# Performance work log

Measured on AMD Instinct MI355X. Metric: run time of the kernel, lower is better.

Reference implementation:

```python
import jax, jax.numpy as jnp
import numpy as np

EMBED_TIME = 128
NUM_HEADS = 4
INPUT_DIM = 64
NHIDDEN = 256
B, LQ, LK = 4, 256, 512


def setup_inputs() -> dict:
    key = jax.random.key(0)
    ks = jax.random.split(key, 8)
    scale = np.float32(0.05)
    return {
        "query": jax.random.normal(ks[0], (B, LQ, EMBED_TIME), jnp.float32),
        "key_ts": jax.random.normal(ks[1], (B, LK, EMBED_TIME), jnp.float32),
        "value": jax.random.normal(ks[2], (B, LK, INPUT_DIM), jnp.float32),
        "mask": jax.random.randint(ks[3], (B, LK, INPUT_DIM), 0, 2, jnp.int32),
        # params stored [in, out] (transpose of torch nn.Linear convention)
        "Wq": jax.random.normal(ks[4], (EMBED_TIME, EMBED_TIME), jnp.float32) * scale,
        "bq": jnp.zeros((EMBED_TIME,), jnp.float32),
        "Wk": jax.random.normal(ks[5], (EMBED_TIME, EMBED_TIME), jnp.float32) * scale,
        "bk": jnp.zeros((EMBED_TIME,), jnp.float32),
        "W3": jax.random.normal(ks[6], (INPUT_DIM * NUM_HEADS, NHIDDEN), jnp.float32) * scale,
        "b3": jnp.zeros((NHIDDEN,), jnp.float32),
    }


def reference(query, key_ts, value, mask, Wq, bq, Wk, bk, W3, b3):
    b, lk, d = value.shape  # B, Lk, input_dim
    h = NUM_HEADS
    dk = EMBED_TIME // h
    # project & split heads: [B, L, E] -> [B, h, L, dk]
    q = (query @ Wq + bq).reshape(b, -1, h, dk).transpose(0, 2, 1, 3)
    k = (key_ts @ Wk + bk).reshape(b, -1, h, dk).transpose(0, 2, 1, 3)
    # scaled dot-product time scores: [B, h, Lq, Lk]
    scores = jnp.einsum('bhqe,bhke->bhqk', q, k) / np.float32(np.sqrt(dk))
    # broadcast scores over value feature dim, mask per feature: [B, h, Lq, Lk, D]
    scores = jnp.where(mask[:, None, None, :, :] == 0, jnp.float32(-1e9), scores[..., None])
    # softmax over key (time) axis, per feature
    p_attn = jax.nn.softmax(scores, axis=-2)
    # elementwise weighted reduce over Lk: [B, h, Lq, D]
    x = jnp.einsum('bhqkd,bkd->bhqd', p_attn, value)
    x = x.transpose(0, 2, 1, 3).reshape(b, -1, h * d)  # [B, Lq, h*D]
    # replicate reinitialize_dim: permute input columns of last layer by descending L1 norm
    perm = jnp.argsort(-jnp.sum(jnp.abs(W3), axis=1))
    return x @ W3[perm] + b3
```

## Files before the change

kernel.cpp:

```cpp
#include <hip/hip_runtime.h>
#include <math.h>

#define ETIME 128
#define NHEADS 4
#define DK 32
#define DIN 64
#define NHID 256
#define BB 4
#define LQg 256
#define LKg 512
#define KC 128
#define KCN 4
#define QT 16

__global__ __launch_bounds__(256) void prep_all(
    const float* __restrict__ query, const float* __restrict__ key_ts,
    const float* __restrict__ Wq, const float* __restrict__ bq,
    const float* __restrict__ Wk, const float* __restrict__ bk,
    const float* __restrict__ value, const int* __restrict__ mask,
    const float* __restrict__ W3,
    float* __restrict__ qbuf, float* __restrict__ kbuf,
    float2* __restrict__ vmbuf, float* __restrict__ sbuf)
{
    __shared__ float in_lds[8][ETIME];
    __shared__ float red[4];
    const int t = threadIdx.x;
    const int blk = blockIdx.x;

    if (blk < 384) {
        const int r0 = blk * 8;
        const bool is_q = (r0 < BB * LQg);
        const float* in   = is_q ? (query + (size_t)r0 * ETIME)
                                 : (key_ts + (size_t)(r0 - BB * LQg) * ETIME);
        const float* W    = is_q ? Wq : Wk;
        const float* bias = is_q ? bq : bk;
        float* outp       = is_q ? (qbuf + (size_t)r0 * ETIME)
                                 : (kbuf + (size_t)(r0 - BB * LQg) * ETIME);

        reinterpret_cast<float4*>(&in_lds[0][0])[t] =
            reinterpret_cast<const float4*>(in)[t];
        __syncthreads();

        const int j4 = t & 31;
        const int row = t >> 5;
        const float4* W4 = reinterpret_cast<const float4*>(W);
        float4 acc = make_float4(0.f, 0.f, 0.f, 0.f);
#pragma unroll 8
        for (int i = 0; i < ETIME; ++i) {
            const float4 w = W4[i * 32 + j4];
            const float xv = in_lds[row][i];
            acc.x = fmaf(xv, w.x, acc.x);
            acc.y = fmaf(xv, w.y, acc.y);
            acc.z = fmaf(xv, w.z, acc.z);
            acc.w = fmaf(xv, w.w, acc.w);
        }
        const float4 bb = reinterpret_cast<const float4*>(bias)[j4];
        acc.x += bb.x; acc.y += bb.y; acc.z += bb.z; acc.w += bb.w;
        reinterpret_cast<float4*>(outp + row * ETIME)[j4] = acc;
    } else if (blk < 640) {
        const int i = (blk - 384) * 256 + t;
        for (int idx = i; idx < BB * LKg * DIN; idx += 256 * 256) {
            const float mf = (float)mask[idx];
            vmbuf[idx] = make_float2(mf, value[idx] * mf);
        }
    } else {
        const int row = blk - 640;
        float a = fabsf(W3[(size_t)row * NHID + t]);
#pragma unroll
        for (int off = 32; off; off >>= 1) a += __shfl_xor(a, off, 64);
        if ((t & 63) == 0) red[t >> 6] = a;
        __syncthreads();
        if (t == 0) sbuf[row] = red[0] + red[1] + red[2] + red[3];
    }
}

__global__ __launch_bounds__(256, 4) void attn_chunk(
    const float* __restrict__ qbuf, const float* __restrict__ kbuf,
    const float2* __restrict__ vmbuf, float2* __restrict__ pbuf)
{
    __shared__ float qlds[QT][DK];
    __shared__ float S[QT][KC];

    const int t = threadIdx.x;
    int bid = blockIdx.x;
    bid = (bid & 7) * 128 + (bid >> 3);
    const int kc = bid & 3;
    const int qt = (bid >> 2) & 15;
    const int h  = (bid >> 6) & 3;
    const int b  = bid >> 8;
    const int qbase = qt * QT;
    const int kbase = kc * KC;

    if (t < 128) {
        const int q = t >> 3, j = t & 7;
        float4 v = reinterpret_cast<const float4*>(
            qbuf + (size_t)(b * LQg + qbase + q) * ETIME + h * DK)[j];
        const float rsq = 0.17677669529663687f;
        v.x *= rsq; v.y *= rsq; v.z *= rsq; v.w *= rsq;
        reinterpret_cast<float4*>(&qlds[q][0])[j] = v;
    }
    __syncthreads();

    {
        const int k = t & 127;
        const int qg = t >> 7;
        const float* krow = kbuf + (size_t)(b * LKg + kbase + k) * ETIME + h * DK;
        float4 kr[8];
#pragma unroll
        for (int i = 0; i < 8; ++i)
            kr[i] = reinterpret_cast<const float4*>(krow)[i];
        float acc[8] = {0, 0, 0, 0, 0, 0, 0, 0};
#pragma unroll
        for (int i4 = 0; i4 < 8; ++i4) {
            const float4 kv = kr[i4];
#pragma unroll
            for (int jj = 0; jj < 8; ++jj) {
                const float4 qv =
                    reinterpret_cast<const float4*>(&qlds[qg * 8 + jj][0])[i4];
                acc[jj] = fmaf(qv.x, kv.x, acc[jj]);
                acc[jj] = fmaf(qv.y, kv.y, acc[jj]);
                acc[jj] = fmaf(qv.z, kv.z, acc[jj]);
                acc[jj] = fmaf(qv.w, kv.w, acc[jj]);
            }
        }
#pragma unroll
        for (int jj = 0; jj < 8; ++jj)
            S[qg * 8 + jj][k] = __expf(acc[jj]);
    }
    __syncthreads();

    {
        const int d = t & 63;
        const int w = t >> 6;
        float num[4] = {0, 0, 0, 0}, den[4] = {0, 0, 0, 0};
        const float2* vp = vmbuf + (size_t)(b * LKg + kbase) * DIN + d;
#pragma unroll 4
        for (int k4 = 0; k4 < KC / 4; ++k4) {
            float2 vm[4];
#pragma unroll
            for (int u = 0; u < 4; ++u) vm[u] = vp[(size_t)(k4 * 4 + u) * DIN];
#pragma unroll
            for (int jj = 0; jj < 4; ++jj) {
                const float4 e4 =
                    reinterpret_cast<const float4*>(&S[w * 4 + jj][0])[k4];
                num[jj] = fmaf(e4.x, vm[0].y, num[jj]); den[jj] = fmaf(e4.x, vm[0].x, den[jj]);
                num[jj] = fmaf(e4.y, vm[1].y, num[jj]); den[jj] = fmaf(e4.y, vm[1].x, den[jj]);
                num[jj] = fmaf(e4.z, vm[2].y, num[jj]); den[jj] = fmaf(e4.z, vm[2].x, den[jj]);
                num[jj] = fmaf(e4.w, vm[3].y, num[jj]); den[jj] = fmaf(e4.w, vm[3].x, den[jj]);
            }
        }
#pragma unroll
        for (int jj = 0; jj < 4; ++jj) {
            const int q = qbase + w * 4 + jj;
            pbuf[((size_t)((b * NHEADS + h) * LQg + q) * KCN + kc) * DIN + d] =
                make_float2(den[jj], num[jj]);
        }
    }
}

__global__ __launch_bounds__(256) void out_fused(
    const float2* __restrict__ pbuf, const float* __restrict__ W3,
    const float* __restrict__ b3, const float* __restrict__ sbuf,
    float* __restrict__ out)
{
    __shared__ float s_lds[NHID];
    __shared__ float xraw[4][NHID];
    __shared__ float x2[4][NHID];
    const int t = threadIdx.x;
    const int r0 = blockIdx.x * 4;
    const int b = r0 >> 8;
    const int q0 = r0 & 255;
    const int h = t >> 6, d = t & 63;

    s_lds[t] = sbuf[t];
#pragma unroll
    for (int r = 0; r < 4; ++r) {
        const float2* pp =
            pbuf + ((size_t)((b * NHEADS + h) * LQg + q0 + r) * KCN) * DIN + d;
        float num = 0.f, den = 0.f;
#pragma unroll
        for (int kc = 0; kc < KCN; ++kc) {
            const float2 v = pp[kc * DIN];
            den += v.x; num += v.y;
        }
        xraw[r][t] = num / den;
    }
    __syncthreads();

    const float si = s_lds[t];
    int rank = 0;
#pragma unroll 8
    for (int j = 0; j < NHID; ++j) {
        const float sj = s_lds[j];
        rank += (sj > si) || (sj == si && j < t);
    }
#pragma unroll
    for (int r = 0; r < 4; ++r) x2[r][t] = xraw[r][rank];
    __syncthreads();

    float acc[4] = {0, 0, 0, 0};
#pragma unroll 4
    for (int c4 = 0; c4 < NHID / 4; ++c4) {
        const float w0 = W3[(size_t)(c4 * 4 + 0) * NHID + t];
        const float w1 = W3[(size_t)(c4 * 4 + 1) * NHID + t];
        const float w2 = W3[(size_t)(c4 * 4 + 2) * NHID + t];
        const float w3 = W3[(size_t)(c4 * 4 + 3) * NHID + t];
#pragma unroll
        for (int r = 0; r < 4; ++r) {
            const float4 xv = reinterpret_cast<const float4*>(&x2[r][0])[c4];
            acc[r] = fmaf(xv.x, w0, acc[r]);
            acc[r] = fmaf(xv.y, w1, acc[r]);
            acc[r] = fmaf(xv.z, w2, acc[r]);
            acc[r] = fmaf(xv.w, w3, acc[r]);
        }
    }
    const float bn = b3[t];
#pragma unroll
    for (int r = 0; r < 4; ++r) out[(size_t)(r0 + r) * NHID + t] = acc[r] + bn;
}

extern "C" void kernel_launch(void* const* d_in, const int* in_sizes, int n_in,
                              void* d_out, int out_size, void* d_ws, size_t ws_size,
                              hipStream_t stream) {
    const float* query  = (const float*)d_in[0];
    const float* key_ts = (const float*)d_in[1];
    const float* value  = (const float*)d_in[2];
    const int*   mask   = (const int*)d_in[3];
    const float* Wq     = (const float*)d_in[4];
    const float* bq     = (const float*)d_in[5];
    const float* Wk     = (const float*)d_in[6];
    const float* bk     = (const float*)d_in[7];
    const float* W3     = (const float*)d_in[8];
    const float* b3     = (const float*)d_in[9];
    float* out = (float*)d_out;

    char* ws = (char*)d_ws;
    float*  qbuf  = (float*) (ws);
    float*  kbuf  = (float*) (ws + (512u  << 10));
    float2* vmbuf = (float2*)(ws + (1536u << 10));
    float2* pbuf  = (float2*)(ws + (2560u << 10));
    float*  sbuf  = (float*) (ws + (10752u << 10));

    prep_all<<<896, 256, 0, stream>>>(query, key_ts, Wq, bq, Wk, bk,
                                      value, mask, W3, qbuf, kbuf, vmbuf, sbuf);
    attn_chunk<<<BB * NHEADS * QT * KCN, 256, 0, stream>>>(qbuf, kbuf, vmbuf, pbuf);
    out_fused<<<BB * LQg / 4, 256, 0, stream>>>(pbuf, W3, b3, sbuf, out);
}
```

Baseline: 51.43 us.

## Head-major q/k layout, LDS-staged keys, split-K value reduce, tiled output GEMM

The prep kernel now writes q and k projections in a head-major [B,H,L,DK] layout, so attention blocks read contiguous tiles. Those blocks stage keys through padded LDS. The value reduction is reorganised so each wave owns 32 keys across all 16 queries, and the partial sums are combined in shared memory before one store. The output kernel moves to 512 threads, stages W3 through LDS in 32-row tiles with register prefetch, and computes two rows per thread. Costs are higher register pressure in attn_chunk (occupancy hint drops to 3) and more LDS use.

```diff
diff --git a/kernel.cpp b/kernel.cpp
--- a/kernel.cpp
+++ b/kernel.cpp
@@ -34,8 +34,6 @@
                                  : (key_ts + (size_t)(r0 - BB * LQg) * ETIME);
         const float* W    = is_q ? Wq : Wk;
         const float* bias = is_q ? bq : bk;
-        float* outp       = is_q ? (qbuf + (size_t)r0 * ETIME)
-                                 : (kbuf + (size_t)(r0 - BB * LQg) * ETIME);
 
         reinterpret_cast<float4*>(&in_lds[0][0])[t] =
             reinterpret_cast<const float4*>(in)[t];
@@ -56,7 +54,17 @@
         }
         const float4 bb = reinterpret_cast<const float4*>(bias)[j4];
         acc.x += bb.x; acc.y += bb.y; acc.z += bb.z; acc.w += bb.w;
-        reinterpret_cast<float4*>(outp + row * ETIME)[j4] = acc;
+
+        const int h = j4 >> 3, dd = (j4 & 7) * 4;
+        float* dst;
+        if (is_q) {
+            const int gr = r0 + row, b = gr >> 8, q = gr & 255;
+            dst = qbuf + ((size_t)((b * NHEADS + h) * LQg + q)) * DK + dd;
+        } else {
+            const int gr = r0 - BB * LQg + row, b = gr >> 9, k = gr & 511;
+            dst = kbuf + ((size_t)((b * NHEADS + h) * LKg + k)) * DK + dd;
+        }
+        *reinterpret_cast<float4*>(dst) = acc;
     } else if (blk < 640) {
         const int i = (blk - 384) * 256 + t;
         for (int idx = i; idx < BB * LKg * DIN; idx += 256 * 256) {
@@ -74,12 +82,15 @@
     }
 }
 
-__global__ __launch_bounds__(256, 4) void attn_chunk(
+__global__ __launch_bounds__(256, 3) void attn_chunk(
     const float* __restrict__ qbuf, const float* __restrict__ kbuf,
     const float2* __restrict__ vmbuf, float2* __restrict__ pbuf)
 {
+    __shared__ float smem[4 * QT * DIN * 2];
+    __shared__ float S[QT][KC];
     __shared__ float qlds[QT][DK];
-    __shared__ float S[QT][KC];
+    float (*klds)[33] = reinterpret_cast<float(*)[33]>(smem);
+    float2 (*xpart)[QT][DIN] = reinterpret_cast<float2(*)[QT][DIN]>(smem);
 
     const int t = threadIdx.x;
     int bid = blockIdx.x;
@@ -92,35 +103,43 @@
     const int kbase = kc * KC;
 
     if (t < 128) {
-        const int q = t >> 3, j = t & 7;
         float4 v = reinterpret_cast<const float4*>(
-            qbuf + (size_t)(b * LQg + qbase + q) * ETIME + h * DK)[j];
+            qbuf + ((size_t)((b * NHEADS + h) * LQg + qbase)) * DK)[t];
         const float rsq = 0.17677669529663687f;
         v.x *= rsq; v.y *= rsq; v.z *= rsq; v.w *= rsq;
-        reinterpret_cast<float4*>(&qlds[q][0])[j] = v;
+        reinterpret_cast<float4*>(&qlds[t >> 3][0])[t & 7] = v;
+    }
+    {
+        const float4* ksrc = reinterpret_cast<const float4*>(
+            kbuf + ((size_t)((b * NHEADS + h) * LKg + kbase)) * DK);
+#pragma unroll
+        for (int u = 0; u < 4; ++u) {
+            const int idx4 = t + u * 256;
+            const float4 v = ksrc[idx4];
+            const int k = idx4 >> 3, c = (idx4 & 7) * 4;
+            klds[k][c + 0] = v.x; klds[k][c + 1] = v.y;
+            klds[k][c + 2] = v.z; klds[k][c + 3] = v.w;
+        }
     }
     __syncthreads();
 
     {
         const int k = t & 127;
         const int qg = t >> 7;
-        const float* krow = kbuf + (size_t)(b * LKg + kbase + k) * ETIME + h * DK;
-        float4 kr[8];
-#pragma unroll
-        for (int i = 0; i < 8; ++i)
-            kr[i] = reinterpret_cast<const float4*>(krow)[i];
+        float kr[DK];
+#pragma unroll
+        for (int i = 0; i < DK; ++i) kr[i] = klds[k][i];
         float acc[8] = {0, 0, 0, 0, 0, 0, 0, 0};
 #pragma unroll
         for (int i4 = 0; i4 < 8; ++i4) {
-            const float4 kv = kr[i4];
 #pragma unroll
             for (int jj = 0; jj < 8; ++jj) {
                 const float4 qv =
                     reinterpret_cast<const float4*>(&qlds[qg * 8 + jj][0])[i4];
-                acc[jj] = fmaf(qv.x, kv.x, acc[jj]);
-                acc[jj] = fmaf(qv.y, kv.y, acc[jj]);
-                acc[jj] = fmaf(qv.z, kv.z, acc[jj]);
-                acc[jj] = fmaf(qv.w, kv.w, acc[jj]);
+                acc[jj] = fmaf(qv.x, kr[i4 * 4 + 0], acc[jj]);
+                acc[jj] = fmaf(qv.y, kr[i4 * 4 + 1], acc[jj]);
+                acc[jj] = fmaf(qv.z, kr[i4 * 4 + 2], acc[jj]);
+                acc[jj] = fmaf(qv.w, kr[i4 * 4 + 3], acc[jj]);
             }
         }
 #pragma unroll
@@ -132,33 +151,37 @@
     {
         const int d = t & 63;
         const int w = t >> 6;
-        float num[4] = {0, 0, 0, 0}, den[4] = {0, 0, 0, 0};
-        const float2* vp = vmbuf + (size_t)(b * LKg + kbase) * DIN + d;
-#pragma unroll 4
-        for (int k4 = 0; k4 < KC / 4; ++k4) {
-            float2 vm[4];
-#pragma unroll
-            for (int u = 0; u < 4; ++u) vm[u] = vp[(size_t)(k4 * 4 + u) * DIN];
-#pragma unroll
-            for (int jj = 0; jj < 4; ++jj) {
-                const float4 e4 =
-                    reinterpret_cast<const float4*>(&S[w * 4 + jj][0])[k4];
-                num[jj] = fmaf(e4.x, vm[0].y, num[jj]); den[jj] = fmaf(e4.x, vm[0].x, den[jj]);
-                num[jj] = fmaf(e4.y, vm[1].y, num[jj]); den[jj] = fmaf(e4.y, vm[1].x, den[jj]);
-                num[jj] = fmaf(e4.z, vm[2].y, num[jj]); den[jj] = fmaf(e4.z, vm[2].x, den[jj]);
-                num[jj] = fmaf(e4.w, vm[3].y, num[jj]); den[jj] = fmaf(e4.w, vm[3].x, den[jj]);
+        const float2* vp = vmbuf + ((size_t)(b * LKg + kbase + w * 32)) * DIN + d;
+        float2 vm[32];
+#pragma unroll
+        for (int u = 0; u < 32; ++u) vm[u] = vp[(size_t)u * DIN];
+#pragma unroll 2
+        for (int q = 0; q < QT; ++q) {
+            const float4* Sq = reinterpret_cast<const float4*>(&S[q][w * 32]);
+            float num = 0.f, den = 0.f;
+#pragma unroll
+            for (int k4 = 0; k4 < 8; ++k4) {
+                const float4 e = Sq[k4];
+                num = fmaf(e.x, vm[k4 * 4 + 0].y, num); den = fmaf(e.x, vm[k4 * 4 + 0].x, den);
+                num = fmaf(e.y, vm[k4 * 4 + 1].y, num); den = fmaf(e.y, vm[k4 * 4 + 1].x, den);
+                num = fmaf(e.z, vm[k4 * 4 + 2].y, num); den = fmaf(e.z, vm[k4 * 4 + 2].x, den);
+                num = fmaf(e.w, vm[k4 * 4 + 3].y, num); den = fmaf(e.w, vm[k4 * 4 + 3].x, den);
             }
-        }
-#pragma unroll
-        for (int jj = 0; jj < 4; ++jj) {
-            const int q = qbase + w * 4 + jj;
-            pbuf[((size_t)((b * NHEADS + h) * LQg + q) * KCN + kc) * DIN + d] =
-                make_float2(den[jj], num[jj]);
-        }
-    }
-}
-
-__global__ __launch_bounds__(256) void out_fused(
+            xpart[w][q][d] = make_float2(den, num);
+        }
+    }
+    __syncthreads();
+
+    for (int e = t; e < QT * DIN; e += 256) {
+        const int q = e >> 6, d = e & 63;
+        const float2 p0 = xpart[0][q][d], p1 = xpart[1][q][d];
+        const float2 p2 = xpart[2][q][d], p3 = xpart[3][q][d];
+        pbuf[((size_t)((b * NHEADS + h) * LQg + qbase + q) * KCN + kc) * DIN + d] =
+            make_float2(p0.x + p1.x + p2.x + p3.x, p0.y + p1.y + p2.y + p3.y);
+    }
+}
+
+__global__ __launch_bounds__(512) void out_fused(
     const float2* __restrict__ pbuf, const float* __restrict__ W3,
     const float* __restrict__ b3, const float* __restrict__ sbuf,
     float* __restrict__ out)
@@ -166,15 +189,18 @@
     __shared__ float s_lds[NHID];
     __shared__ float xraw[4][NHID];
     __shared__ float x2[4][NHID];
+    __shared__ float W3l[32][NHID];
     const int t = threadIdx.x;
     const int r0 = blockIdx.x * 4;
     const int b = r0 >> 8;
     const int q0 = r0 & 255;
-    const int h = t >> 6, d = t & 63;
-
-    s_lds[t] = sbuf[t];
-#pragma unroll
-    for (int r = 0; r < 4; ++r) {
+
+    if (t < NHID) s_lds[t] = sbuf[t];
+#pragma unroll
+    for (int u = 0; u < 2; ++u) {
+        const int e = t + u * 512;
+        const int r = e >> 8, c = e & 255;
+        const int h = c >> 6, d = c & 63;
         const float2* pp =
             pbuf + ((size_t)((b * NHEADS + h) * LQg + q0 + r) * KCN) * DIN + d;
         float num = 0.f, den = 0.f;
@@ -183,40 +209,57 @@
             const float2 v = pp[kc * DIN];
             den += v.x; num += v.y;
         }
-        xraw[r][t] = num / den;
-    }
-    __syncthreads();
-
-    const float si = s_lds[t];
-    int rank = 0;
+        xraw[r][c] = num / den;
+    }
+    __syncthreads();
+
+    if (t < NHID) {
+        const float si = s_lds[t];
+        int rank = 0;
 #pragma unroll 8
-    for (int j = 0; j < NHID; ++j) {
-        const float sj = s_lds[j];
-        rank += (sj > si) || (sj == si && j < t);
-    }
-#pragma unroll
-    for (int r = 0; r < 4; ++r) x2[r][t] = xraw[r][rank];
-    __syncthreads();
-
-    float acc[4] = {0, 0, 0, 0};
-#pragma unroll 4
-    for (int c4 = 0; c4 < NHID / 4; ++c4) {
-        const float w0 = W3[(size_t)(c4 * 4 + 0) * NHID + t];
-        const float w1 = W3[(size_t)(c4 * 4 + 1) * NHID + t];
-        const float w2 = W3[(size_t)(c4 * 4 + 2) * NHID + t];
-        const float w3 = W3[(size_t)(c4 * 4 + 3) * NHID + t];
-#pragma unroll
-        for (int r = 0; r < 4; ++r) {
-            const float4 xv = reinterpret_cast<const float4*>(&x2[r][0])[c4];
-            acc[r] = fmaf(xv.x, w0, acc[r]);
-            acc[r] = fmaf(xv.y, w1, acc[r]);
-            acc[r] = fmaf(xv.z, w2, acc[r]);
-            acc[r] = fmaf(xv.w, w3, acc[r]);
-        }
-    }
-    const float bn = b3[t];
-#pragma unroll
-    for (int r = 0; r < 4; ++r) out[(size_t)(r0 + r) * NHID + t] = acc[r] + bn;
+        for (int j = 0; j < NHID; ++j) {
+            const float sj = s_lds[j];
+            rank += (sj > si) || (sj == si && j < t);
+        }
+#pragma unroll
+        for (int r = 0; r < 4; ++r) x2[r][t] = xraw[r][rank];
+    }
+
+    const int n = t & 255, rh = t >> 8;
+    const float4* W3g4 = reinterpret_cast<const float4*>(W3);
+    float4 pf[4];
+#pragma unroll
+    for (int u = 0; u < 4; ++u) pf[u] = W3g4[t + u * 512];
+    float acc0 = 0.f, acc1 = 0.f;
+
+    for (int kt = 0; kt < 8; ++kt) {
+        __syncthreads();
+#pragma unroll
+        for (int u = 0; u < 4; ++u)
+            reinterpret_cast<float4*>(&W3l[0][0])[t + u * 512] = pf[u];
+        if (kt < 7) {
+#pragma unroll
+            for (int u = 0; u < 4; ++u)
+                pf[u] = W3g4[(kt + 1) * 2048 + t + u * 512];
+        }
+        __syncthreads();
+#pragma unroll
+        for (int c4 = 0; c4 < 8; ++c4) {
+            const float4 xa = *reinterpret_cast<const float4*>(&x2[2 * rh][kt * 32 + c4 * 4]);
+            const float4 xb = *reinterpret_cast<const float4*>(&x2[2 * rh + 1][kt * 32 + c4 * 4]);
+            const float w0 = W3l[c4 * 4 + 0][n];
+            const float w1 = W3l[c4 * 4 + 1][n];
+            const float w2 = W3l[c4 * 4 + 2][n];
+            const float w3 = W3l[c4 * 4 + 3][n];
+            acc0 = fmaf(xa.x, w0, acc0); acc1 = fmaf(xb.x, w0, acc1);
+            acc0 = fmaf(xa.y, w1, acc0); acc1 = fmaf(xb.y, w1, acc1);
+            acc0 = fmaf(xa.z, w2, acc0); acc1 = fmaf(xb.z, w2, acc1);
+            acc0 = fmaf(xa.w, w3, acc0); acc1 = fmaf(xb.w, w3, acc1);
+        }
+    }
+    const float bn = b3[n];
+    out[(size_t)(r0 + 2 * rh + 0) * NHID + n] = acc0 + bn;
+    out[(size_t)(r0 + 2 * rh + 1) * NHID + n] = acc1 + bn;
 }
 
 extern "C" void kernel_launch(void* const* d_in, const int* in_sizes, int n_in,
@@ -244,5 +287,5 @@
     prep_all<<<896, 256, 0, stream>>>(query, key_ts, Wq, bq, Wk, bk,
                                       value, mask, W3, qbuf, kbuf, vmbuf, sbuf);
     attn_chunk<<<BB * NHEADS * QT * KCN, 256, 0, stream>>>(qbuf, kbuf, vmbuf, pbuf);
-    out_fused<<<BB * LQg / 4, 256, 0, stream>>>(pbuf, W3, b3, sbuf, out);
-}
+    out_fused<<<BB * LQg / 4, 512, 0, stream>>>(pbuf, W3, b3, sbuf, out);
+}
```

Measured after the change: 62.16 us. +20.9%, slower.

## Bit-pack mask, halve key chunk, stage K in LDS, split output GEMV

Applied to the files above, without the earlier changes.

The mask is packed into 64-bit ballot words and value is pre-masked, which replaces the float2 value/mask buffer and cuts the bytes read in the attention reduce. The key chunk shrinks from 128 to 64, doubling the attention grid to 2048 blocks, and K rows are staged in padded LDS. The value loads are software-prefetched one step ahead. The output kernel moves to 512 threads that split the hidden reduction in half and combine the halves through LDS, at the cost of a larger partial buffer and more partial sums to reduce.

```diff
diff --git a/kernel.cpp b/kernel.cpp
--- a/kernel.cpp
+++ b/kernel.cpp
@@ -9,9 +9,11 @@
 #define BB 4
 #define LQg 256
 #define LKg 512
-#define KC 128
-#define KCN 4
+#define KC 64
+#define KCN 8
 #define QT 16
+
+typedef unsigned long long ull;
 
 __global__ __launch_bounds__(256) void prep_all(
     const float* __restrict__ query, const float* __restrict__ key_ts,
@@ -20,7 +22,7 @@
     const float* __restrict__ value, const int* __restrict__ mask,
     const float* __restrict__ W3,
     float* __restrict__ qbuf, float* __restrict__ kbuf,
-    float2* __restrict__ vmbuf, float* __restrict__ sbuf)
+    float* __restrict__ valm, ull* __restrict__ mbits, float* __restrict__ sbuf)
 {
     __shared__ float in_lds[8][ETIME];
     __shared__ float red[4];
@@ -58,10 +60,16 @@
         acc.x += bb.x; acc.y += bb.y; acc.z += bb.z; acc.w += bb.w;
         reinterpret_cast<float4*>(outp + row * ETIME)[j4] = acc;
     } else if (blk < 640) {
-        const int i = (blk - 384) * 256 + t;
-        for (int idx = i; idx < BB * LKg * DIN; idx += 256 * 256) {
-            const float mf = (float)mask[idx];
-            vmbuf[idx] = make_float2(mf, value[idx] * mf);
+        const int lane = t & 63;
+        const int wgid = (blk - 384) * 4 + (t >> 6);
+#pragma unroll
+        for (int u = 0; u < 2; ++u) {
+            const int p = wgid * 2 + u;
+            const int idx = p * 64 + lane;
+            const int m = mask[idx];
+            valm[idx] = m ? value[idx] : 0.f;
+            const ull bits = __ballot(m != 0);
+            if (lane == 0) mbits[p] = bits;
         }
     } else {
         const int row = blk - 640;
@@ -76,18 +84,20 @@
 
 __global__ __launch_bounds__(256, 4) void attn_chunk(
     const float* __restrict__ qbuf, const float* __restrict__ kbuf,
-    const float2* __restrict__ vmbuf, float2* __restrict__ pbuf)
+    const float* __restrict__ valm, const ull* __restrict__ mbits,
+    float2* __restrict__ pbuf)
 {
     __shared__ float qlds[QT][DK];
+    __shared__ float klds[KC][DK + 1];
     __shared__ float S[QT][KC];
 
     const int t = threadIdx.x;
     int bid = blockIdx.x;
-    bid = (bid & 7) * 128 + (bid >> 3);
-    const int kc = bid & 3;
-    const int qt = (bid >> 2) & 15;
-    const int h  = (bid >> 6) & 3;
-    const int b  = bid >> 8;
+    bid = (bid & 7) * 256 + (bid >> 3);
+    const int kc = bid & 7;
+    const int qt = (bid >> 3) & 15;
+    const int h  = (bid >> 7) & 3;
+    const int b  = bid >> 9;
     const int qbase = qt * QT;
     const int kbase = kc * KC;
 
@@ -99,33 +109,42 @@
         v.x *= rsq; v.y *= rsq; v.z *= rsq; v.w *= rsq;
         reinterpret_cast<float4*>(&qlds[q][0])[j] = v;
     }
-    __syncthreads();
-
     {
-        const int k = t & 127;
-        const int qg = t >> 7;
-        const float* krow = kbuf + (size_t)(b * LKg + kbase + k) * ETIME + h * DK;
-        float4 kr[8];
-#pragma unroll
-        for (int i = 0; i < 8; ++i)
-            kr[i] = reinterpret_cast<const float4*>(krow)[i];
-        float acc[8] = {0, 0, 0, 0, 0, 0, 0, 0};
+#pragma unroll
+        for (int u = 0; u < 2; ++u) {
+            const int idx4 = t + u * 256;
+            const int k = idx4 >> 3, c = idx4 & 7;
+            const float4 v = reinterpret_cast<const float4*>(
+                kbuf + (size_t)(b * LKg + kbase + k) * ETIME + h * DK)[c];
+            klds[k][c * 4 + 0] = v.x; klds[k][c * 4 + 1] = v.y;
+            klds[k][c * 4 + 2] = v.z; klds[k][c * 4 + 3] = v.w;
+        }
+    }
+    __syncthreads();
+
+    {
+        const int k = t & 63;
+        const int qg = t >> 6;
+        float acc[4] = {0, 0, 0, 0};
 #pragma unroll
         for (int i4 = 0; i4 < 8; ++i4) {
-            const float4 kv = kr[i4];
-#pragma unroll
-            for (int jj = 0; jj < 8; ++jj) {
+            float kr0 = klds[k][i4 * 4 + 0];
+            float kr1 = klds[k][i4 * 4 + 1];
+            float kr2 = klds[k][i4 * 4 + 2];
+            float kr3 = klds[k][i4 * 4 + 3];
+#pragma unroll
+            for (int jj = 0; jj < 4; ++jj) {
                 const float4 qv =
-                    reinterpret_cast<const float4*>(&qlds[qg * 8 + jj][0])[i4];
-                acc[jj] = fmaf(qv.x, kv.x, acc[jj]);
-                acc[jj] = fmaf(qv.y, kv.y, acc[jj]);
-                acc[jj] = fmaf(qv.z, kv.z, acc[jj]);
-                acc[jj] = fmaf(qv.w, kv.w, acc[jj]);
+                    reinterpret_cast<const float4*>(&qlds[qg * 4 + jj][0])[i4];
+                acc[jj] = fmaf(qv.x, kr0, acc[jj]);
+                acc[jj] = fmaf(qv.y, kr1, acc[jj]);
+                acc[jj] = fmaf(qv.z, kr2, acc[jj]);
+                acc[jj] = fmaf(qv.w, kr3, acc[jj]);
             }
         }
 #pragma unroll
-        for (int jj = 0; jj < 8; ++jj)
-            S[qg * 8 + jj][k] = __expf(acc[jj]);
+        for (int jj = 0; jj < 4; ++jj)
+            S[qg * 4 + jj][k] = __expf(acc[jj]);
     }
     __syncthreads();
 
@@ -133,21 +152,34 @@
         const int d = t & 63;
         const int w = t >> 6;
         float num[4] = {0, 0, 0, 0}, den[4] = {0, 0, 0, 0};
-        const float2* vp = vmbuf + (size_t)(b * LKg + kbase) * DIN + d;
-#pragma unroll 4
+        const float* vp = valm + (size_t)(b * LKg + kbase) * DIN + d;
+        const ull*   mp = mbits + b * LKg + kbase;
+        float vcur[4], vnxt[4];
+#pragma unroll
+        for (int u = 0; u < 4; ++u) vcur[u] = vp[(size_t)u * DIN];
         for (int k4 = 0; k4 < KC / 4; ++k4) {
-            float2 vm[4];
-#pragma unroll
-            for (int u = 0; u < 4; ++u) vm[u] = vp[(size_t)(k4 * 4 + u) * DIN];
+            if (k4 < KC / 4 - 1) {
+#pragma unroll
+                for (int u = 0; u < 4; ++u)
+                    vnxt[u] = vp[(size_t)((k4 + 1) * 4 + u) * DIN];
+            }
+            ull mb[4];
+#pragma unroll
+            for (int u = 0; u < 4; ++u) mb[u] = mp[k4 * 4 + u];
+            float mf[4];
+#pragma unroll
+            for (int u = 0; u < 4; ++u) mf[u] = (float)((mb[u] >> d) & 1ull);
 #pragma unroll
             for (int jj = 0; jj < 4; ++jj) {
-                const float4 e4 =
-                    reinterpret_cast<const float4*>(&S[w * 4 + jj][0])[k4];
-                num[jj] = fmaf(e4.x, vm[0].y, num[jj]); den[jj] = fmaf(e4.x, vm[0].x, den[jj]);
-                num[jj] = fmaf(e4.y, vm[1].y, num[jj]); den[jj] = fmaf(e4.y, vm[1].x, den[jj]);
-                num[jj] = fmaf(e4.z, vm[2].y, num[jj]); den[jj] = fmaf(e4.z, vm[2].x, den[jj]);
-                num[jj] = fmaf(e4.w, vm[3].y, num[jj]); den[jj] = fmaf(e4.w, vm[3].x, den[jj]);
+                const float4 e =
+                    *reinterpret_cast<const float4*>(&S[w * 4 + jj][k4 * 4]);
+                num[jj] = fmaf(e.x, vcur[0], num[jj]); den[jj] = fmaf(e.x, mf[0], den[jj]);
+                num[jj] = fmaf(e.y, vcur[1], num[jj]); den[jj] = fmaf(e.y, mf[1], den[jj]);
+                num[jj] = fmaf(e.z, vcur[2], num[jj]); den[jj] = fmaf(e.z, mf[2], den[jj]);
+                num[jj] = fmaf(e.w, vcur[3], num[jj]); den[jj] = fmaf(e.w, mf[3], den[jj]);
             }
+#pragma unroll
+            for (int u = 0; u < 4; ++u) vcur[u] = vnxt[u];
         }
 #pragma unroll
         for (int jj = 0; jj < 4; ++jj) {
@@ -158,7 +190,7 @@
     }
 }
 
-__global__ __launch_bounds__(256) void out_fused(
+__global__ __launch_bounds__(512) void out_fused(
     const float2* __restrict__ pbuf, const float* __restrict__ W3,
     const float* __restrict__ b3, const float* __restrict__ sbuf,
     float* __restrict__ out)
@@ -166,15 +198,18 @@
     __shared__ float s_lds[NHID];
     __shared__ float xraw[4][NHID];
     __shared__ float x2[4][NHID];
+    __shared__ float redl[4][NHID];
     const int t = threadIdx.x;
     const int r0 = blockIdx.x * 4;
     const int b = r0 >> 8;
     const int q0 = r0 & 255;
-    const int h = t >> 6, d = t & 63;
-
-    s_lds[t] = sbuf[t];
-#pragma unroll
-    for (int r = 0; r < 4; ++r) {
+
+    if (t < NHID) s_lds[t] = sbuf[t];
+#pragma unroll
+    for (int u = 0; u < 2; ++u) {
+        const int e = t + u * 512;
+        const int r = e >> 8, c = e & 255;
+        const int h = c >> 6, d = c & 63;
         const float2* pp =
             pbuf + ((size_t)((b * NHEADS + h) * LQg + q0 + r) * KCN) * DIN + d;
         float num = 0.f, den = 0.f;
@@ -183,40 +218,53 @@
             const float2 v = pp[kc * DIN];
             den += v.x; num += v.y;
         }
-        xraw[r][t] = num / den;
-    }
-    __syncthreads();
-
-    const float si = s_lds[t];
-    int rank = 0;
+        xraw[r][c] = num / den;
+    }
+    __syncthreads();
+
+    if (t < NHID) {
+        const float si = s_lds[t];
+        int rank = 0;
 #pragma unroll 8
-    for (int j = 0; j < NHID; ++j) {
-        const float sj = s_lds[j];
-        rank += (sj > si) || (sj == si && j < t);
-    }
-#pragma unroll
-    for (int r = 0; r < 4; ++r) x2[r][t] = xraw[r][rank];
-    __syncthreads();
-
+        for (int j = 0; j < NHID; ++j) {
+            const float sj = s_lds[j];
+            rank += (sj > si) || (sj == si && j < t);
+        }
+#pragma unroll
+        for (int r = 0; r < 4; ++r) x2[r][t] = xraw[r][rank];
+    }
+    __syncthreads();
+
+    const int n = t & 255, half = t >> 8;
+    const int c0 = half * 128;
     float acc[4] = {0, 0, 0, 0};
-#pragma unroll 4
-    for (int c4 = 0; c4 < NHID / 4; ++c4) {
-        const float w0 = W3[(size_t)(c4 * 4 + 0) * NHID + t];
-        const float w1 = W3[(size_t)(c4 * 4 + 1) * NHID + t];
-        const float w2 = W3[(size_t)(c4 * 4 + 2) * NHID + t];
-        const float w3 = W3[(size_t)(c4 * 4 + 3) * NHID + t];
+#pragma unroll 8
+    for (int c4 = 0; c4 < 32; ++c4) {
+        const int c = c0 + c4 * 4;
+        const float w0 = W3[(size_t)(c + 0) * NHID + n];
+        const float w1 = W3[(size_t)(c + 1) * NHID + n];
+        const float w2 = W3[(size_t)(c + 2) * NHID + n];
+        const float w3 = W3[(size_t)(c + 3) * NHID + n];
 #pragma unroll
         for (int r = 0; r < 4; ++r) {
-            const float4 xv = reinterpret_cast<const float4*>(&x2[r][0])[c4];
+            const float4 xv = *reinterpret_cast<const float4*>(&x2[r][c]);
             acc[r] = fmaf(xv.x, w0, acc[r]);
             acc[r] = fmaf(xv.y, w1, acc[r]);
             acc[r] = fmaf(xv.z, w2, acc[r]);
             acc[r] = fmaf(xv.w, w3, acc[r]);
         }
     }
-    const float bn = b3[t];
-#pragma unroll
-    for (int r = 0; r < 4; ++r) out[(size_t)(r0 + r) * NHID + t] = acc[r] + bn;
+    if (half == 1) {
+#pragma unroll
+        for (int r = 0; r < 4; ++r) redl[r][n] = acc[r];
+    }
+    __syncthreads();
+    if (t < NHID) {
+        const float bn = b3[n];
+#pragma unroll
+        for (int r = 0; r < 4; ++r)
+            out[(size_t)(r0 + r) * NHID + n] = acc[r] + redl[r][n] + bn;
+    }
 }
 
 extern "C" void kernel_launch(void* const* d_in, const int* in_sizes, int n_in,
@@ -236,13 +284,14 @@
 
     char* ws = (char*)d_ws;
     float*  qbuf  = (float*) (ws);
-    float*  kbuf  = (float*) (ws + (512u  << 10));
-    float2* vmbuf = (float2*)(ws + (1536u << 10));
-    float2* pbuf  = (float2*)(ws + (2560u << 10));
-    float*  sbuf  = (float*) (ws + (10752u << 10));
+    float*  kbuf  = (float*) (ws + (512u   << 10));
+    float*  valm  = (float*) (ws + (1536u  << 10));
+    float2* pbuf  = (float2*)(ws + (2048u  << 10));
+    ull*    mbits = (ull*)   (ws + (18432u << 10));
+    float*  sbuf  = (float*) (ws + (18448u << 10));
 
     prep_all<<<896, 256, 0, stream>>>(query, key_ts, Wq, bq, Wk, bk,
-                                      value, mask, W3, qbuf, kbuf, vmbuf, sbuf);
-    attn_chunk<<<BB * NHEADS * QT * KCN, 256, 0, stream>>>(qbuf, kbuf, vmbuf, pbuf);
-    out_fused<<<BB * LQg / 4, 256, 0, stream>>>(pbuf, W3, b3, sbuf, out);
-}
+                                      value, mask, W3, qbuf, kbuf, valm, mbits, sbuf);
+    attn_chunk<<<BB * NHEADS * QT * KCN, 256, 0, stream>>>(qbuf, kbuf, valm, mbits, pbuf);
+    out_fused<<<BB * LQg / 4, 512, 0, stream>>>(pbuf, W3, b3, sbuf, out);
+}
```

New measurement: 63.16 us. +22.8%, slower.
